# Kernel optimization log

Hardware: AMD Instinct MI355X
Metric: run time of the kernel (lower is better)

## Reference

```python
import jax, jax.numpy as jnp
import numpy as np

N = 2_000_000
FX, FY, CX, CY = 1111.0, 1111.0, 960.0, 540.0


def setup_inputs() -> dict:
    key = jax.random.key(0)
    k1, k2, k3, k4 = jax.random.split(key, 4)
    xy = jax.random.normal(k1, (N, 2), jnp.float32) * 2.0
    z = jax.random.uniform(k2, (N, 1), jnp.float32, 2.0, 10.0)  # positive world z
    points = jnp.concatenate([xy, z], axis=1)
    quaternions = jax.random.normal(k3, (N, 4), jnp.float32)
    scales = jax.random.uniform(k4, (N, 3), jnp.float32, 0.01, 0.1)
    # realistic pinhole camera: small rotation about y + translation, depth stays positive
    th = 0.1
    R = np.array([[np.cos(th), 0.0, np.sin(th)],
                  [0.0, 1.0, 0.0],
                  [-np.sin(th), 0.0, np.cos(th)]], dtype=np.float32)
    t = np.array([0.1, -0.2, 1.0], dtype=np.float32)
    extrinsic = np.eye(4, dtype=np.float32)
    extrinsic[:3, :3] = R
    extrinsic[:3, 3] = t
    intrinsic = np.array([[FX, 0.0, CX, 0.0],
                          [0.0, FY, CY, 0.0],
                          [0.0, 0.0, 1.0, 0.0]], dtype=np.float32)
    return {
        "points": points,
        "quaternions": quaternions,
        "scales": scales,
        "extrinsic_matrix": jnp.asarray(extrinsic),
        "intrinsic_matrix": jnp.asarray(intrinsic),
    }


def _quat_to_rotmat(q):
    # COLMAP qvec2rotmat convention: q = (w, x, y, z), q assumed normalized. -> (N,3,3)
    w, x, y, z = q[:, 0], q[:, 1], q[:, 2], q[:, 3]
    r0 = jnp.stack([1 - 2 * (y * y + z * z), 2 * (x * y - w * z), 2 * (x * z + w * y)], axis=-1)
    r1 = jnp.stack([2 * (x * y + w * z), 1 - 2 * (x * x + z * z), 2 * (y * z - w * x)], axis=-1)
    r2 = jnp.stack([2 * (x * z - w * y), 2 * (y * z + w * x), 1 - 2 * (x * x + y * y)], axis=-1)
    return jnp.stack([r0, r1, r2], axis=1)


def reference(points, quaternions, scales, extrinsic_matrix, intrinsic_matrix):
    n = points.shape[0]
    # --- 3D covariance: Sigma = (R diag(s)) (R diag(s))^T ---
    q = quaternions / jnp.linalg.norm(quaternions, axis=1, keepdims=True)
    R = _quat_to_rotmat(q)                       # (N,3,3)
    M = R * scales[:, None, :]                   # R @ diag(s): scale columns
    cov3d = jnp.einsum('nij,nkj->nik', M, M)     # (N,3,3)
    # --- project points to camera then image plane ---
    ones = jnp.ones((n, 1), points.dtype)
    pts_h = jnp.concatenate([points, ones], axis=1)          # (N,4)
    cam = pts_h @ extrinsic_matrix.T                         # (N,4) camera coords
    cam3 = cam[:, :3] / cam[:, 3:4]                          # perspective-normalized camera coords
    z_component = cam[:, 2:3]                                # (N,1)
    proj = jnp.concatenate([cam3, ones], axis=1) @ intrinsic_matrix.T  # (N,3)
    projected_points = proj[:, :2] / proj[:, 2:3]            # (N,2)
    # --- 2D covariance: T = J W^T, cov2d = (T Sigma T^T)[:2,:2] ---
    fx = intrinsic_matrix[0, 0]
    fy = intrinsic_matrix[1, 1]
    # getWorld2View(R,t) has [:3,:3] = R^T; W ends up as extrinsic[:3,:3]^T
    W = extrinsic_matrix[:3, :3].T
    cx, cy, cz = cam3[:, 0], cam3[:, 1], cam3[:, 2]
    zeros = jnp.zeros_like(cz)
    J = jnp.stack([
        jnp.stack([fx / cz, zeros, -fx * cx / (cz * cz)], axis=-1),
        jnp.stack([zeros, fy / cz, -fy * cy / (cz * cz)], axis=-1),
        jnp.stack([zeros, zeros, zeros], axis=-1),
    ], axis=1)                                               # (N,3,3)
    T = jnp.einsum('nij,kj->nik', J, W)                      # J @ W^T
    T2 = T[:, :2, :]                                         # only top 2 rows matter
    projected_covariance = jnp.einsum('nij,njk,nlk->nil', T2, cov3d, T2)  # (N,2,2)
    return projected_points, z_component, projected_covariance
```

## Files before the change

kernel.cpp:

```cpp
#include <hip/hip_runtime.h>
#include <cstdint>

typedef float v4f __attribute__((ext_vector_type(4)));

__device__ __forceinline__ float frcp(float x) {
    float r = __builtin_amdgcn_rcpf(x);
    return r * (2.0f - x * r);
}
__device__ __forceinline__ float frsq(float x) {
    float r = __builtin_amdgcn_rsqf(x);
    return r * (1.5f - 0.5f * x * r * r);
}

struct POut { float u, v, zc, o00, o01, o10, o11; };

__global__ __launch_bounds__(256) void gs_project_kernel(
    const float* __restrict__ points,
    const float* __restrict__ quats,
    const float* __restrict__ scales,
    const float* __restrict__ E,
    const float* __restrict__ K,
    float* __restrict__ out,
    int n)
{
    const int t = blockIdx.x * blockDim.x + threadIdx.x;
    const long long i0 = (long long)t * 4;
    if (i0 >= n) return;

    const float e00=E[0],  e01=E[1],  e02=E[2],  e03=E[3];
    const float e10=E[4],  e11=E[5],  e12=E[6],  e13=E[7];
    const float e20=E[8],  e21=E[9],  e22=E[10], e23=E[11];
    const float e30=E[12], e31=E[13], e32=E[14], e33=E[15];
    const float k00=K[0],  k01=K[1],  k02=K[2],  k03=K[3];
    const float k10=K[4],  k11=K[5],  k12=K[6],  k13=K[7];
    const float k20=K[8],  k21=K[9],  k22=K[10], k23=K[11];

    auto project = [&](float px, float py, float pz,
                       float qw, float qx, float qy, float qz_,
                       float sx, float sy, float sz) -> POut
    {
        const float qi = frsq(qw*qw + qx*qx + qy*qy + qz_*qz_);
        const float w = qw*qi, x = qx*qi, y = qy*qi, z = qz_*qi;

        const float r00 = 1.f - 2.f*(y*y + z*z);
        const float r01 = 2.f*(x*y - w*z);
        const float r02 = 2.f*(x*z + w*y);
        const float r10 = 2.f*(x*y + w*z);
        const float r11 = 1.f - 2.f*(x*x + z*z);
        const float r12 = 2.f*(y*z - w*x);
        const float r20 = 2.f*(x*z - w*y);
        const float r21 = 2.f*(y*z + w*x);
        const float r22 = 1.f - 2.f*(x*x + y*y);

        const float m00=r00*sx, m01=r01*sy, m02=r02*sz;
        const float m10=r10*sx, m11=r11*sy, m12=r12*sz;
        const float m20=r20*sx, m21=r21*sy, m22=r22*sz;

        const float c00 = m00*m00 + m01*m01 + m02*m02;
        const float c01 = m00*m10 + m01*m11 + m02*m12;
        const float c02 = m00*m20 + m01*m21 + m02*m22;
        const float c11 = m10*m10 + m11*m11 + m12*m12;
        const float c12 = m10*m20 + m11*m21 + m12*m22;
        const float c22 = m20*m20 + m21*m21 + m22*m22;

        const float camx = e00*px + e01*py + e02*pz + e03;
        const float camy = e10*px + e11*py + e12*pz + e13;
        const float camz = e20*px + e21*py + e22*pz + e23;
        const float camw = e30*px + e31*py + e32*pz + e33;
        const float iw = frcp(camw);
        const float cx = camx*iw, cy = camy*iw, cz = camz*iw;

        const float p0 = k00*cx + k01*cy + k02*cz + k03;
        const float p1 = k10*cx + k11*cy + k12*cz + k13;
        const float p2 = k20*cx + k21*cy + k22*cz + k23;
        const float ip2 = frcp(p2);

        const float fx = k00, fy = k11;
        const float icz = frcp(cz);
        const float j00 = fx*icz;
        const float j02 = -fx*cx*icz*icz;
        const float j11 = fy*icz;
        const float j12 = -fy*cy*icz*icz;

        const float t00 = j00*e00 + j02*e20;
        const float t01 = j00*e01 + j02*e21;
        const float t02 = j00*e02 + j02*e22;
        const float t10 = j11*e10 + j12*e20;
        const float t11 = j11*e11 + j12*e21;
        const float t12 = j11*e12 + j12*e22;

        const float a00 = t00*c00 + t01*c01 + t02*c02;
        const float a01 = t00*c01 + t01*c11 + t02*c12;
        const float a02 = t00*c02 + t01*c12 + t02*c22;
        const float a10 = t10*c00 + t11*c01 + t12*c02;
        const float a11 = t10*c01 + t11*c11 + t12*c12;
        const float a12 = t10*c02 + t11*c12 + t12*c22;

        POut o;
        o.u  = p0*ip2;
        o.v  = p1*ip2;
        o.zc = camz;
        o.o00 = a00*t00 + a01*t01 + a02*t02;
        o.o01 = a00*t10 + a01*t11 + a02*t12;
        o.o10 = a10*t00 + a11*t01 + a12*t02;
        o.o11 = a10*t10 + a11*t11 + a12*t12;
        return o;
    };

    if (((n & 3) == 0) && (i0 + 3 < n)) {
        const v4f* p4 = (const v4f*)points + 3*(size_t)t;
        const v4f* q4 = (const v4f*)quats  + 4*(size_t)t;
        const v4f* s4 = (const v4f*)scales + 3*(size_t)t;

        const v4f P0 = p4[0], P1 = p4[1], P2 = p4[2];
        const v4f Q0 = q4[0], Q1 = q4[1], Q2 = q4[2], Q3 = q4[3];
        const v4f S0 = s4[0], S1 = s4[1], S2 = s4[2];

        const POut r0 = project(P0.x, P0.y, P0.z,  Q0.x, Q0.y, Q0.z, Q0.w,  S0.x, S0.y, S0.z);
        const POut r1 = project(P0.w, P1.x, P1.y,  Q1.x, Q1.y, Q1.z, Q1.w,  S0.w, S1.x, S1.y);
        const POut r2 = project(P1.z, P1.w, P2.x,  Q2.x, Q2.y, Q2.z, Q2.w,  S1.z, S1.w, S2.x);
        const POut r3 = project(P2.y, P2.z, P2.w,  Q3.x, Q3.y, Q3.z, Q3.w,  S2.y, S2.z, S2.w);

        const v4f U0 = {r0.u, r0.v, r1.u, r1.v};
        const v4f U1 = {r2.u, r2.v, r3.u, r3.v};
        const v4f Z  = {r0.zc, r1.zc, r2.zc, r3.zc};
        const v4f C0 = {r0.o00, r0.o01, r0.o10, r0.o11};
        const v4f C1 = {r1.o00, r1.o01, r1.o10, r1.o11};
        const v4f C2 = {r2.o00, r2.o01, r2.o10, r2.o11};
        const v4f C3 = {r3.o00, r3.o01, r3.o10, r3.o11};

        v4f* uvout = (v4f*)out + 2*(size_t)t;
        uvout[0] = U0;
        uvout[1] = U1;

        v4f* zout = (v4f*)(out + 2*(size_t)n) + t;
        zout[0] = Z;

        v4f* cout = (v4f*)(out + 3*(size_t)n) + (size_t)i0;
        cout[0] = C0; cout[1] = C1; cout[2] = C2; cout[3] = C3;
    } else {
        for (long long i = i0; i < n && i < i0 + 4; ++i) {
            const POut r = project(points[3*i+0], points[3*i+1], points[3*i+2],
                                   quats[4*i+0], quats[4*i+1], quats[4*i+2], quats[4*i+3],
                                   scales[3*i+0], scales[3*i+1], scales[3*i+2]);
            out[2*i+0] = r.u; out[2*i+1] = r.v;
            out[2*(size_t)n + i] = r.zc;
            float* cov_out = out + 3*(size_t)n + 4*i;
            cov_out[0] = r.o00; cov_out[1] = r.o01; cov_out[2] = r.o10; cov_out[3] = r.o11;
        }
    }
}

extern "C" void kernel_launch(void* const* d_in, const int* in_sizes, int n_in,
                              void* d_out, int out_size, void* d_ws, size_t ws_size,
                              hipStream_t stream) {
    const float* points = (const float*)d_in[0];
    const float* quats  = (const float*)d_in[1];
    const float* scales = (const float*)d_in[2];
    const float* E      = (const float*)d_in[3];
    const float* K      = (const float*)d_in[4];
    float* out = (float*)d_out;

    const int n = in_sizes[0] / 3;
    const int threads = (n + 3) / 4;
    const int block = 256;
    const int grid = (threads + block - 1) / block;
    gs_project_kernel<<<grid, block, 0, stream>>>(points, quats, scales, E, K, out, n);
}
```

Measured before the change: 138.6 us.

## Stage points and scales through LDS for coalesced per-lane element processing

Each 256-thread block now handles 1024 elements. It first cooperatively copies the point and scale arrays into shared memory with fully coalesced vec4 loads, then each lane processes one element per iteration, so adjacent lanes touch adjacent elements and every global load and store is coalesced. Before, each thread handled 4 consecutive elements, which gave strided vec4 accesses across lanes. The change adds an LDS round-trip and a block barrier, and it has a three-way strided LDS read pattern that may cause bank conflicts.

Result: faster. 126.3 us (-8.9%).

```diff
diff --git a/kernel.cpp b/kernel.cpp
--- a/kernel.cpp
+++ b/kernel.cpp
@@ -2,6 +2,7 @@
 #include <cstdint>
 
 typedef float v4f __attribute__((ext_vector_type(4)));
+typedef float v2f __attribute__((ext_vector_type(2)));
 
 __device__ __forceinline__ float frcp(float x) {
     float r = __builtin_amdgcn_rcpf(x);
@@ -23,9 +24,13 @@
     float* __restrict__ out,
     int n)
 {
-    const int t = blockIdx.x * blockDim.x + threadIdx.x;
-    const long long i0 = (long long)t * 4;
-    if (i0 >= n) return;
+    const int tid  = threadIdx.x;
+    const int lane = tid & 63;
+    const int wv   = tid >> 6;
+    const long long blockBase = (long long)blockIdx.x * 1024;
+
+    __shared__ float lds_p[3072];
+    __shared__ float lds_s[3072];
 
     const float e00=E[0],  e01=E[1],  e02=E[2],  e03=E[3];
     const float e10=E[4],  e11=E[5],  e12=E[6],  e13=E[7];
@@ -107,39 +112,43 @@
         return o;
     };
 
-    if (((n & 3) == 0) && (i0 + 3 < n)) {
-        const v4f* p4 = (const v4f*)points + 3*(size_t)t;
-        const v4f* q4 = (const v4f*)quats  + 4*(size_t)t;
-        const v4f* s4 = (const v4f*)scales + 3*(size_t)t;
+    if (blockBase + 1024 <= n) {
+        const v4f* gp = (const v4f*)points + (size_t)blockIdx.x * 768;
+        const v4f* gs = (const v4f*)scales + (size_t)blockIdx.x * 768;
+        v4f* lp = (v4f*)lds_p;
+        v4f* ls = (v4f*)lds_s;
+        #pragma unroll
+        for (int m = 0; m < 3; ++m) {
+            lp[tid + 256*m] = gp[tid + 256*m];
+            ls[tid + 256*m] = gs[tid + 256*m];
+        }
+        __syncthreads();
 
-        const v4f P0 = p4[0], P1 = p4[1], P2 = p4[2];
-        const v4f Q0 = q4[0], Q1 = q4[1], Q2 = q4[2], Q3 = q4[3];
-        const v4f S0 = s4[0], S1 = s4[1], S2 = s4[2];
+        const long long waveBase = blockBase + 256*wv;
+        const int lbase = 256*wv;
 
-        const POut r0 = project(P0.x, P0.y, P0.z,  Q0.x, Q0.y, Q0.z, Q0.w,  S0.x, S0.y, S0.z);
-        const POut r1 = project(P0.w, P1.x, P1.y,  Q1.x, Q1.y, Q1.z, Q1.w,  S0.w, S1.x, S1.y);
-        const POut r2 = project(P1.z, P1.w, P2.x,  Q2.x, Q2.y, Q2.z, Q2.w,  S1.z, S1.w, S2.x);
-        const POut r3 = project(P2.y, P2.z, P2.w,  Q3.x, Q3.y, Q3.z, Q3.w,  S2.y, S2.z, S2.w);
+        const v4f* gq = (const v4f*)quats;
+        v2f* uvout = (v2f*)out;
+        float* zout = out + 2*(size_t)n;
+        v4f* cout = (v4f*)(out + 3*(size_t)n);
 
-        const v4f U0 = {r0.u, r0.v, r1.u, r1.v};
-        const v4f U1 = {r2.u, r2.v, r3.u, r3.v};
-        const v4f Z  = {r0.zc, r1.zc, r2.zc, r3.zc};
-        const v4f C0 = {r0.o00, r0.o01, r0.o10, r0.o11};
-        const v4f C1 = {r1.o00, r1.o01, r1.o10, r1.o11};
-        const v4f C2 = {r2.o00, r2.o01, r2.o10, r2.o11};
-        const v4f C3 = {r3.o00, r3.o01, r3.o10, r3.o11};
+        #pragma unroll
+        for (int k = 0; k < 4; ++k) {
+            const long long p = waveBase + 64*k + lane;
+            const int pl = 3*(lbase + 64*k + lane);
 
-        v4f* uvout = (v4f*)out + 2*(size_t)t;
-        uvout[0] = U0;
-        uvout[1] = U1;
+            const v4f q = gq[p];
+            const float px = lds_p[pl+0], py = lds_p[pl+1], pz = lds_p[pl+2];
+            const float sx = lds_s[pl+0], sy = lds_s[pl+1], sz = lds_s[pl+2];
 
-        v4f* zout = (v4f*)(out + 2*(size_t)n) + t;
-        zout[0] = Z;
+            const POut r = project(px, py, pz, q.x, q.y, q.z, q.w, sx, sy, sz);
 
-        v4f* cout = (v4f*)(out + 3*(size_t)n) + (size_t)i0;
-        cout[0] = C0; cout[1] = C1; cout[2] = C2; cout[3] = C3;
+            uvout[p] = (v2f){r.u, r.v};
+            zout[p]  = r.zc;
+            cout[p]  = (v4f){r.o00, r.o01, r.o10, r.o11};
+        }
     } else {
-        for (long long i = i0; i < n && i < i0 + 4; ++i) {
+        for (long long i = blockBase + tid; i < n; i += 256) {
             const POut r = project(points[3*i+0], points[3*i+1], points[3*i+2],
                                    quats[4*i+0], quats[4*i+1], quats[4*i+2], quats[4*i+3],
                                    scales[3*i+0], scales[3*i+1], scales[3*i+2]);
@@ -162,8 +171,7 @@
     float* out = (float*)d_out;
 
     const int n = in_sizes[0] / 3;
-    const int threads = (n + 3) / 4;
     const int block = 256;
-    const int grid = (threads + block - 1) / block;
+    const int grid = (n + 1023) / 1024;
     gs_project_kernel<<<grid, block, 0, stream>>>(points, quats, scales, E, K, out, n);
 }
```
